# Performance work log

Measured on AMD Instinct MI355X. Metric: run time of the kernel, lower is better.

## Reference

```python
import jax, jax.numpy as jnp
import numpy as np

B, Q, D = 8, 128, 2048
H, HD = 16, 128           # num_heads, head_dim (D == H*HD)
CACHE = 3968              # tokens already in KV cache; CACHE+Q == max_seq_len


def setup_inputs() -> dict:
    key = jax.random.key(0)
    ks = jax.random.split(key, 6)
    x = jax.random.normal(ks[0], (B, Q, D), dtype=jnp.float32)
    k_cache = jax.random.normal(ks[1], (B, H, CACHE, HD), dtype=jnp.float32)
    v_cache = jax.random.normal(ks[2], (B, H, CACHE, HD), dtype=jnp.float32)
    Wqkv = jax.random.normal(ks[3], (D, 3 * D), dtype=jnp.float32) * 0.02
    Wproj = jax.random.normal(ks[4], (D, D), dtype=jnp.float32) * 0.02
    bproj = jnp.zeros((D,), dtype=jnp.float32)
    return {"x": x, "k_cache": k_cache, "v_cache": v_cache,
            "Wqkv": Wqkv, "Wproj": Wproj, "bproj": bproj}


def reference(x, k_cache, v_cache, Wqkv, Wproj, bproj):
    # QKV projection (qkv_bias=False)
    qkv = x @ Wqkv                                   # [B, Q, 3D]
    qkv = qkv.reshape(B, Q, 3, H, HD)
    qkv = jnp.transpose(qkv, (2, 0, 3, 1, 4))        # [3, B, H, Q, HD]
    q, k_new, v_new = qkv[0], qkv[1], qkv[2]
    # KV-cache append (cache_pos + Q == max_seq_len, no roll)
    k_all = jnp.concatenate([k_cache, k_new], axis=2)  # [B, H, K, HD]
    v_all = jnp.concatenate([v_cache, v_new], axis=2)
    K = CACHE + Q
    scale = 1.0 / jnp.sqrt(jnp.float32(HD))
    scores = jnp.einsum('bhqd,bhkd->bhqk', q, k_all) * scale  # [B, H, Q, K]
    # Causal mask aligned to cache (bottom-right): query i sees keys j <= i + (K - Q)
    i = jnp.arange(Q)[:, None]
    j = jnp.arange(K)[None, :]
    mask = j > (i + (K - Q))
    scores = jnp.where(mask, jnp.float32(-jnp.inf), scores)
    attn = jax.nn.softmax(scores, axis=-1)
    out = jnp.einsum('bhqk,bhkd->bhqd', attn, v_all)   # [B, H, Q, HD]
    out = jnp.transpose(out, (0, 2, 1, 3)).reshape(B, Q, D)
    return out @ Wproj + bproj
```

## Files before the change

### kernel.cpp

```cpp
#include <hip/hip_runtime.h>

typedef unsigned int u32;
typedef unsigned short u16;
typedef short s16x8 __attribute__((ext_vector_type(8)));
typedef float f32x4 __attribute__((ext_vector_type(4)));

#define MFMA16(a,b,c) __builtin_amdgcn_mfma_f32_16x16x32_bf16((a),(b),(c),0,0,0)

#define Bb 8
#define Hh 16
#define Qq 128
#define HDd 128
#define Dd 2048
#define CACHE 3968
#define NSPLIT 4
#define SCALE 0.08838834764831845f
#define SM_OFF 8.0f

__device__ __forceinline__ u16 f2bf(float x){
  u32 u = __builtin_bit_cast(u32, x);
  u32 r = ((u >> 16) & 1u) + 0x7fffu;
  return (u16)((u + r) >> 16);
}
__device__ __forceinline__ float bf2f(u16 h){
  return __builtin_bit_cast(float, ((u32)h) << 16);
}
__device__ __forceinline__ u32 pk2(float a, float b){
  return (u32)f2bf(a) | ((u32)f2bf(b) << 16);
}
__device__ __forceinline__ u32 cvtpk(float a, float b){
  u32 r;
  asm("v_cvt_pk_bf16_f32 %0, %1, %2" : "=v"(r) : "v"(a), "v"(b));
  return r;
}
__device__ __forceinline__ float f4c(const float4& v, int j){
  return j==0 ? v.x : j==1 ? v.y : j==2 ? v.z : v.w;
}
__device__ __forceinline__ void gload_lds16(const void* g, void* l){
  __builtin_amdgcn_global_load_lds(
      (const __attribute__((address_space(1))) u32*)g,
      (__attribute__((address_space(3))) u32*)l, 16, 0, 0);
}
__device__ __forceinline__ void lgkm_barrier(){
  asm volatile("s_waitcnt lgkmcnt(0)" ::: "memory");
  __builtin_amdgcn_s_barrier();
}

__global__ void k_cvt(const float* __restrict__ s, u16* __restrict__ d, int n4){
  int i = blockIdx.x * 256 + threadIdx.x;
  if (i < n4){
    float4 v = *(const float4*)(s + (size_t)i * 4);
    *(uint2*)(d + (size_t)i * 4) = make_uint2(pk2(v.x, v.y), pk2(v.z, v.w));
  }
}

__global__ void k_tcvt(const float* __restrict__ s, u16* __restrict__ d, int R, int C){
  __shared__ float t[32][33];
  int tx = threadIdx.x & 31, ty = threadIdx.x >> 5;
  int c0 = blockIdx.x * 32, r0 = blockIdx.y * 32;
#pragma unroll
  for (int i = 0; i < 4; i++)
    t[ty + i*8][tx] = s[(size_t)(r0 + ty + i*8) * C + c0 + tx];
  __syncthreads();
#pragma unroll
  for (int i = 0; i < 4; i++)
    d[(size_t)(c0 + ty + i*8) * R + r0 + tx] = f2bf(t[tx][ty + i*8]);
}

template<int MODE>
__global__ __launch_bounds__(256)
void k_gemm(const u16* __restrict__ A, const u16* __restrict__ Bt, int K, int N,
            u16* __restrict__ oq, u16* __restrict__ ok, u16* __restrict__ ov,
            float* __restrict__ of, const float* __restrict__ bias)
{
  const int m0 = blockIdx.y * 128, n0 = blockIdx.x * 128;
  const int tid = threadIdx.x;
  const int w = tid >> 6, l = tid & 63;
  const int lg = l >> 4, lr = l & 15;
  const int wr = w >> 1, wc = w & 1;

  __shared__ u16 As[2][128 * 32];
  __shared__ u16 Bs[2][128 * 32];

  f32x4 acc[4][4];
#pragma unroll
  for (int i = 0; i < 4; i++)
#pragma unroll
    for (int j = 0; j < 4; j++) acc[i][j] = f32x4{0.f, 0.f, 0.f, 0.f};

  const int nt = K >> 5;

  auto stage = [&](int buf, int t){
    const int k0 = t << 5;
#pragma unroll
    for (int i = 0; i < 2; i++){
      int flat = i * 256 + tid;
      int row = flat >> 2, kq = flat & 3;
      const u16* ga = A + (size_t)(m0 + row) * K + k0 + kq * 8;
      gload_lds16(ga, (char*)&As[buf][0] + (size_t)(i*256 + w*64) * 16);
      const u16* gb = Bt + (size_t)(n0 + row) * K + k0 + kq * 8;
      gload_lds16(gb, (char*)&Bs[buf][0] + (size_t)(i*256 + w*64) * 16);
    }
  };

  stage(0, 0);
  asm volatile("s_waitcnt vmcnt(0)" ::: "memory");
  __syncthreads();

  for (int t = 0; t < nt; ++t){
    const int buf = t & 1;
    if (t + 1 < nt) stage(buf ^ 1, t + 1);
    s16x8 af[4], bfr[4];
#pragma unroll
    for (int i = 0; i < 4; i++){
      int row = wr*64 + i*16 + lr;
      af[i] = *(const s16x8*)&As[buf][row*32 + lg*8];
    }
#pragma unroll
    for (int j = 0; j < 4; j++){
      int col = wc*64 + j*16 + lr;
      bfr[j] = *(const s16x8*)&Bs[buf][col*32 + lg*8];
    }
#pragma unroll
    for (int i = 0; i < 4; i++)
#pragma unroll
      for (int j = 0; j < 4; j++)
        acc[i][j] = MFMA16(af[i], bfr[j], acc[i][j]);
    asm volatile("s_waitcnt vmcnt(0)" ::: "memory");
    __syncthreads();
  }

#pragma unroll
  for (int i = 0; i < 4; i++){
#pragma unroll
    for (int j = 0; j < 4; j++){
#pragma unroll
      for (int r = 0; r < 4; r++){
        int m = m0 + wr*64 + i*16 + lg*4 + r;
        int n = n0 + wc*64 + j*16 + lr;
        float v = acc[i][j][r];
        if (MODE == 0){
          int which = n >> 11;
          int h = (n >> 7) & 15, hd = n & 127;
          int b = m >> 7, qi = m & 127;
          size_t idx = (((size_t)(b * Hh + h)) * Qq + qi) * HDd + hd;
          if (which == 0)      oq[idx] = f2bf(v * SCALE);
          else if (which == 1) ok[idx] = f2bf(v);
          else                 ov[idx] = f2bf(v);
        } else {
          of[(size_t)m * N + n] = v + bias[n];
        }
      }
    }
  }
}

__global__ __launch_bounds__(512, 2)
void k_attn(const float* __restrict__ kc, const float* __restrict__ vc,
            const u16* __restrict__ qw, const u16* __restrict__ knw,
            const u16* __restrict__ vnw, float* __restrict__ opart,
            float2* __restrict__ ml)
{
  const int tid = threadIdx.x;
  const int w = tid >> 6, l = tid & 63;
  const int lg = l >> 4, lr = l & 15;

  __shared__ __align__(16) u16 Ks[2][64 * 136];
  __shared__ u32 Vts[2][128 * 32];

  const int rv = tid & 15, c4v = tid >> 4;

  const int vb = blockIdx.x;
  const int bh = vb >> 2;
  const int sg = vb & 3;

  s16x8 qf[4];
  {
    const u16* qp = qw + (((size_t)bh * Qq + w*16 + lr) * HDd);
#pragma unroll
    for (int kk = 0; kk < 4; kk++) qf[kk] = *(const s16x8*)(qp + kk*32 + lg*8);
  }

  f32x4 acc[8];
#pragma unroll
  for (int i = 0; i < 8; i++) acc[i] = f32x4{0.f, 0.f, 0.f, 0.f};
  float lpart = 0.f;

  const float* kbase = kc + (size_t)bh * CACHE * HDd;
  const float* vbase = vc + (size_t)bh * CACHE * HDd;
  const u16* knb = knw + (size_t)bh * Qq * HDd;
  const u16* vnb = vnw + (size_t)bh * Qq * HDd;

  float4 kreg[4], vreg[4];

  auto loadc = [&](int c){
    if (c < 62){
#pragma unroll
      for (int i = 0; i < 4; i++){
        int flat = tid + i*512;
        int row = flat >> 5, c4 = flat & 31;
        kreg[i] = *(const float4*)(kbase + ((size_t)(c*64 + row)) * HDd + c4*4);
      }
#pragma unroll
      for (int a = 0; a < 4; a++)
        vreg[a] = *(const float4*)(vbase + ((size_t)(c*64 + rv + a*16)) * HDd + c4v*4);
    } else {
#pragma unroll
      for (int i = 0; i < 4; i++){
        int flat = tid + i*512;
        int row = flat >> 5, c4 = flat & 31;
        ushort4 u = *(const ushort4*)(knb + ((size_t)(c*64 + row - CACHE)) * HDd + c4*4);
        kreg[i] = make_float4(bf2f(u.x), bf2f(u.y), bf2f(u.z), bf2f(u.w));
      }
#pragma unroll
      for (int a = 0; a < 4; a++){
        ushort4 u = *(const ushort4*)(vnb + ((size_t)(c*64 + rv + a*16 - CACHE)) * HDd + c4v*4);
        vreg[a] = make_float4(bf2f(u.x), bf2f(u.y), bf2f(u.z), bf2f(u.w));
      }
    }
  };

  auto writeK = [&](int buf){
#pragma unroll
    for (int i = 0; i < 4; i++){
      int flat = tid + i*512;
      int row = flat >> 5, c4 = flat & 31;
      *(uint2*)&Ks[buf][row*136 + c4*4] =
          make_uint2(cvtpk(kreg[i].x, kreg[i].y), cvtpk(kreg[i].z, kreg[i].w));
    }
  };
  auto writeV = [&](int buf){
#pragma unroll
    for (int j = 0; j < 4; j++){
      int col = c4v*4 + j;
      int x2 = (col & 7) << 2;
      Vts[buf][col*32 + (rv ^ x2)]        = cvtpk(f4c(vreg[0], j), f4c(vreg[1], j));
      Vts[buf][col*32 + ((rv + 16) ^ x2)] = cvtpk(f4c(vreg[2], j), f4c(vreg[3], j));
    }
  };

  int cur = 0;
  loadc(sg * 16);
  writeK(0);
  writeV(0);
  __syncthreads();

  for (int cl = 0; cl < 16; ++cl){
    const int c = sg * 16 + cl;
    if (cl + 1 < 16) loadc(c + 1);

    f32x4 s[4];
    __builtin_amdgcn_s_setprio(1);
#pragma unroll
    for (int t = 0; t < 4; t++){
      s[t] = f32x4{0.f, 0.f, 0.f, 0.f};
      const u16* kp = &Ks[cur][(t*16 + lr) * 136];
#pragma unroll
      for (int kk = 0; kk < 4; kk++){
        s16x8 kf = *(const s16x8*)(kp + kk*32 + lg*8);
        s[t] = MFMA16(kf, qf[kk], s[t]);
      }
    }
    __builtin_amdgcn_s_setprio(0);

    if (c >= 62){
      int jn = c*64 - CACHE;
      int qi = w*16 + lr;
#pragma unroll
      for (int t = 0; t < 4; t++)
#pragma unroll
        for (int r = 0; r < 4; r++){
          int kn = jn + t*16 + lg*4 + r;
          if (kn > qi) s[t][r] = -__builtin_inff();
        }
    }

    float ps = 0.f;
#pragma unroll
    for (int t = 0; t < 4; t++)
#pragma unroll
      for (int r = 0; r < 4; r++){
        float p = __expf(s[t][r] - SM_OFF);
        s[t][r] = p;
        ps += p;
      }
    lpart += ps;

    s16x8 pf[2];
    {
      union { uint4 u; s16x8 v; } c0, c1;
      c0.u = make_uint4(cvtpk(s[0][0], s[1][0]), cvtpk(s[0][1], s[1][1]),
                        cvtpk(s[0][2], s[1][2]), cvtpk(s[0][3], s[1][3]));
      c1.u = make_uint4(cvtpk(s[2][0], s[3][0]), cvtpk(s[2][1], s[3][1]),
                        cvtpk(s[2][2], s[3][2]), cvtpk(s[2][3], s[3][3]));
      pf[0] = c0.v;
      pf[1] = c1.v;
    }

    if (cl + 1 < 16) writeK(cur ^ 1);

    __builtin_amdgcn_s_setprio(1);
#pragma unroll
    for (int t = 0; t < 8; t++){
      int col = t*16 + lr;
      const u32* vp = &Vts[cur][col * 32];
#pragma unroll
      for (int kk = 0; kk < 2; kk++){
        s16x8 vf = *(const s16x8*)(vp + ((16*kk + 4*lg) ^ ((col & 7) << 2)));
        acc[t] = MFMA16(vf, pf[kk], acc[t]);
      }
    }
    __builtin_amdgcn_s_setprio(0);

    if (cl + 1 < 16) writeV(cur ^ 1);

    lgkm_barrier();
    cur ^= 1;
  }

  float lsum = lpart;
  lsum += __shfl_xor(lsum, 16);
  lsum += __shfl_xor(lsum, 32);

  float* pbase = opart + (size_t)vb * (Qq * HDd);
  float* Lt = (float*)Ks;
#pragma unroll 1
  for (int half = 0; half < 2; half++){
    if ((w >> 2) == half){
      int ql = (w & 3) * 16 + lr;
#pragma unroll
      for (int t = 0; t < 8; t++)
#pragma unroll
        for (int r = 0; r < 4; r++)
          Lt[ql * 132 + t*16 + lg*4 + r] = acc[t][r];
    }
    __syncthreads();
    {
      int c32 = tid & 31;
#pragma unroll
      for (int j = 0; j < 4; j++){
        int ql = (tid >> 5) + j * 16;
        float4 v = *(const float4*)&Lt[ql * 132 + c32 * 4];
        *(float4*)&pbase[(size_t)(half * 64 + ql) * HDd + c32 * 4] = v;
      }
    }
    __syncthreads();
  }
  if (lg == 0)
    ml[(size_t)vb * Qq + w*16 + lr] = make_float2(SM_OFF, lsum);
}

__global__ __launch_bounds__(256)
void k_comb(const float* __restrict__ opart, const float2* __restrict__ ml,
            u16* __restrict__ ao)
{
  const int bh = blockIdx.x >> 2;
  const int q0 = (blockIdx.x & 3) * 32;
  const int tid = threadIdx.x;

  __shared__ float wgt[32][NSPLIT];
  __shared__ float Ls[32];

  if (tid < 32 * NSPLIT){
    int row = tid >> 2, s = tid & 3;
    float2 v = ml[((size_t)(bh * NSPLIT + s)) * Qq + q0 + row];
    float m = v.x;
    m = fmaxf(m, __shfl_xor(m, 1));
    m = fmaxf(m, __shfl_xor(m, 2));
    float e = __expf(v.x - m);
    float el = e * v.y;
    el += __shfl_xor(el, 1);
    el += __shfl_xor(el, 2);
    wgt[row][s] = e;
    if (s == 0) Ls[row] = el;
  }
  __syncthreads();

  const int cp = tid & 63;
  const int r4 = tid >> 6;
  const int b = bh >> 4, h = bh & 15;
#pragma unroll
  for (int rr = 0; rr < 8; rr++){
    int row = r4 + rr*4;
    float2 a = make_float2(0.f, 0.f);
    const float* pb = opart + ((size_t)(bh * NSPLIT)) * (Qq * HDd)
                            + (size_t)(q0 + row) * HDd + cp*2;
#pragma unroll
    for (int s = 0; s < NSPLIT; s++){
      float2 p = *(const float2*)(pb + (size_t)s * (Qq * HDd));
      float wv = wgt[row][s];
      a.x += wv * p.x;
      a.y += wv * p.y;
    }
    float inv = 1.0f / Ls[row];
    u16* dst = ao + ((size_t)b * Qq + q0 + row) * Dd + h * HDd + cp*2;
    *(u32*)dst = pk2(a.x * inv, a.y * inv);
  }
}

extern "C" void kernel_launch(void* const* d_in, const int* in_sizes, int n_in,
                              void* d_out, int out_size, void* d_ws, size_t ws_size,
                              hipStream_t stream)
{
  const float* x     = (const float*)d_in[0];
  const float* kc    = (const float*)d_in[1];
  const float* vc    = (const float*)d_in[2];
  const float* wqkv  = (const float*)d_in[3];
  const float* wproj = (const float*)d_in[4];
  const float* bproj = (const float*)d_in[5];
  float* out = (float*)d_out;

  char* ws = (char*)d_ws;
  u16* xb  = (u16*)(ws);
  u16* wtq = (u16*)(ws + ((size_t)4  << 20));
  u16* wtp = (u16*)(ws + ((size_t)28 << 20));
  u16* qw  = (u16*)(ws + ((size_t)36 << 20));
  u16* knw = (u16*)(ws + ((size_t)40 << 20));
  u16* vnw = (u16*)(ws + ((size_t)44 << 20));
  u16* aow = (u16*)(ws + ((size_t)48 << 20));
  float* opart = (float*)(ws + ((size_t)52 << 20));
  float2* mlw  = (float2*)(ws + ((size_t)116 << 20));

  k_cvt<<<2048, 256, 0, stream>>>(x, xb, (1024 * 2048) / 4);
  k_tcvt<<<dim3(192, 64), 256, 0, stream>>>(wqkv, wtq, 2048, 6144);
  k_tcvt<<<dim3(64, 64), 256, 0, stream>>>(wproj, wtp, 2048, 2048);
  k_gemm<0><<<dim3(48, 8), 256, 0, stream>>>(xb, wtq, 2048, 6144,
                                             qw, knw, vnw, nullptr, nullptr);
  k_attn<<<Bb * Hh * NSPLIT, 512, 0, stream>>>(kc, vc, qw, knw, vnw, opart, mlw);
  k_comb<<<Bb * Hh * 4, 256, 0, stream>>>(opart, mlw, aow);
  k_gemm<1><<<dim3(16, 8), 256, 0, stream>>>(aow, wtp, 2048, 2048,
                                             nullptr, nullptr, nullptr, out, bproj);
}
```

Baseline: 266.9 us.

## Fuse conversion kernels, halve proj GEMM M-tile, drop setprio in attention

Merges the x conversion and both weight transpose-convert kernels into one k_prep launch to cut launch overhead. Templates the GEMM on M-tile size and runs the output projection with 64-row tiles, doubling its grid from 128 to 256 blocks to fill more CUs. Removes s_setprio hints around the MFMA loops in the attention kernel. The smaller tile lowers per-block reuse, and dropping priority may change how waves interleave.

Result: faster. 253.4 us (-5.1%).

```diff
diff --git a/kernel.cpp b/kernel.cpp
--- a/kernel.cpp
+++ b/kernel.cpp
@@ -46,18 +46,25 @@
   __builtin_amdgcn_s_barrier();
 }
 
-__global__ void k_cvt(const float* __restrict__ s, u16* __restrict__ d, int n4){
-  int i = blockIdx.x * 256 + threadIdx.x;
-  if (i < n4){
-    float4 v = *(const float4*)(s + (size_t)i * 4);
-    *(uint2*)(d + (size_t)i * 4) = make_uint2(pk2(v.x, v.y), pk2(v.z, v.w));
-  }
-}
-
-__global__ void k_tcvt(const float* __restrict__ s, u16* __restrict__ d, int R, int C){
+__global__ __launch_bounds__(256)
+void k_prep(const float* __restrict__ x, u16* __restrict__ xb,
+            const float* __restrict__ wqkv, u16* __restrict__ wtq,
+            const float* __restrict__ wproj, u16* __restrict__ wtp)
+{
   __shared__ float t[32][33];
+  int bid = blockIdx.x;
+  if (bid < 2048){
+    int i = bid * 256 + threadIdx.x;
+    float4 v = *(const float4*)(x + (size_t)i * 4);
+    *(uint2*)(xb + (size_t)i * 4) = make_uint2(pk2(v.x, v.y), pk2(v.z, v.w));
+    return;
+  }
+  bid -= 2048;
+  const float* s; u16* d; int R, C, bx, by;
+  if (bid < 12288){ s = wqkv;  d = wtq; R = 2048; C = 6144; bx = bid % 192; by = bid / 192; }
+  else { bid -= 12288; s = wproj; d = wtp; R = 2048; C = 2048; bx = bid % 64;  by = bid / 64;  }
   int tx = threadIdx.x & 31, ty = threadIdx.x >> 5;
-  int c0 = blockIdx.x * 32, r0 = blockIdx.y * 32;
+  int c0 = bx * 32, r0 = by * 32;
 #pragma unroll
   for (int i = 0; i < 4; i++)
     t[ty + i*8][tx] = s[(size_t)(r0 + ty + i*8) * C + c0 + tx];
@@ -67,37 +74,45 @@
     d[(size_t)(c0 + ty + i*8) * R + r0 + tx] = f2bf(t[tx][ty + i*8]);
 }
 
-template<int MODE>
+template<int MODE, int TM>
 __global__ __launch_bounds__(256)
 void k_gemm(const u16* __restrict__ A, const u16* __restrict__ Bt, int K, int N,
             u16* __restrict__ oq, u16* __restrict__ ok, u16* __restrict__ ov,
             float* __restrict__ of, const float* __restrict__ bias)
 {
-  const int m0 = blockIdx.y * 128, n0 = blockIdx.x * 128;
+  const int m0 = blockIdx.y * TM, n0 = blockIdx.x * 128;
   const int tid = threadIdx.x;
   const int w = tid >> 6, l = tid & 63;
   const int lg = l >> 4, lr = l & 15;
-  const int wr = w >> 1, wc = w & 1;
-
-  __shared__ u16 As[2][128 * 32];
+  const int wr = (TM == 128) ? (w >> 1) : 0;
+  const int wc = (TM == 128) ? (w & 1) : w;
+  constexpr int WN = (TM == 128) ? 64 : 32;
+  constexpr int NJ = WN / 16;
+
+  __shared__ u16 As[2][TM * 32];
   __shared__ u16 Bs[2][128 * 32];
 
-  f32x4 acc[4][4];
+  f32x4 acc[4][NJ];
 #pragma unroll
   for (int i = 0; i < 4; i++)
 #pragma unroll
-    for (int j = 0; j < 4; j++) acc[i][j] = f32x4{0.f, 0.f, 0.f, 0.f};
+    for (int j = 0; j < NJ; j++) acc[i][j] = f32x4{0.f, 0.f, 0.f, 0.f};
 
   const int nt = K >> 5;
 
   auto stage = [&](int buf, int t){
     const int k0 = t << 5;
 #pragma unroll
-    for (int i = 0; i < 2; i++){
+    for (int i = 0; i < TM/64; i++){
       int flat = i * 256 + tid;
       int row = flat >> 2, kq = flat & 3;
       const u16* ga = A + (size_t)(m0 + row) * K + k0 + kq * 8;
       gload_lds16(ga, (char*)&As[buf][0] + (size_t)(i*256 + w*64) * 16);
+    }
+#pragma unroll
+    for (int i = 0; i < 2; i++){
+      int flat = i * 256 + tid;
+      int row = flat >> 2, kq = flat & 3;
       const u16* gb = Bt + (size_t)(n0 + row) * K + k0 + kq * 8;
       gload_lds16(gb, (char*)&Bs[buf][0] + (size_t)(i*256 + w*64) * 16);
     }
@@ -110,21 +125,21 @@
   for (int t = 0; t < nt; ++t){
     const int buf = t & 1;
     if (t + 1 < nt) stage(buf ^ 1, t + 1);
-    s16x8 af[4], bfr[4];
+    s16x8 af[4], bfr[NJ];
 #pragma unroll
     for (int i = 0; i < 4; i++){
       int row = wr*64 + i*16 + lr;
       af[i] = *(const s16x8*)&As[buf][row*32 + lg*8];
     }
 #pragma unroll
-    for (int j = 0; j < 4; j++){
-      int col = wc*64 + j*16 + lr;
+    for (int j = 0; j < NJ; j++){
+      int col = wc*WN + j*16 + lr;
       bfr[j] = *(const s16x8*)&Bs[buf][col*32 + lg*8];
     }
 #pragma unroll
     for (int i = 0; i < 4; i++)
 #pragma unroll
-      for (int j = 0; j < 4; j++)
+      for (int j = 0; j < NJ; j++)
         acc[i][j] = MFMA16(af[i], bfr[j], acc[i][j]);
     asm volatile("s_waitcnt vmcnt(0)" ::: "memory");
     __syncthreads();
@@ -133,11 +148,11 @@
 #pragma unroll
   for (int i = 0; i < 4; i++){
 #pragma unroll
-    for (int j = 0; j < 4; j++){
+    for (int j = 0; j < NJ; j++){
 #pragma unroll
       for (int r = 0; r < 4; r++){
         int m = m0 + wr*64 + i*16 + lg*4 + r;
-        int n = n0 + wc*64 + j*16 + lr;
+        int n = n0 + wc*WN + j*16 + lr;
         float v = acc[i][j][r];
         if (MODE == 0){
           int which = n >> 11;
@@ -250,7 +265,6 @@
     if (cl + 1 < 16) loadc(c + 1);
 
     f32x4 s[4];
-    __builtin_amdgcn_s_setprio(1);
 #pragma unroll
     for (int t = 0; t < 4; t++){
       s[t] = f32x4{0.f, 0.f, 0.f, 0.f};
@@ -261,7 +275,6 @@
         s[t] = MFMA16(kf, qf[kk], s[t]);
       }
     }
-    __builtin_amdgcn_s_setprio(0);
 
     if (c >= 62){
       int jn = c*64 - CACHE;
@@ -299,7 +312,6 @@
 
     if (cl + 1 < 16) writeK(cur ^ 1);
 
-    __builtin_amdgcn_s_setprio(1);
 #pragma unroll
     for (int t = 0; t < 8; t++){
       int col = t*16 + lr;
@@ -310,7 +322,6 @@
         acc[t] = MFMA16(vf, pf[kk], acc[t]);
       }
     }
-    __builtin_amdgcn_s_setprio(0);
 
     if (cl + 1 < 16) writeV(cur ^ 1);
 
@@ -421,13 +432,11 @@
   float* opart = (float*)(ws + ((size_t)52 << 20));
   float2* mlw  = (float2*)(ws + ((size_t)116 << 20));
 
-  k_cvt<<<2048, 256, 0, stream>>>(x, xb, (1024 * 2048) / 4);
-  k_tcvt<<<dim3(192, 64), 256, 0, stream>>>(wqkv, wtq, 2048, 6144);
-  k_tcvt<<<dim3(64, 64), 256, 0, stream>>>(wproj, wtp, 2048, 2048);
-  k_gemm<0><<<dim3(48, 8), 256, 0, stream>>>(xb, wtq, 2048, 6144,
-                                             qw, knw, vnw, nullptr, nullptr);
+  k_prep<<<18432, 256, 0, stream>>>(x, xb, wqkv, wtq, wproj, wtp);
+  k_gemm<0,128><<<dim3(48, 8), 256, 0, stream>>>(xb, wtq, 2048, 6144,
+                                                 qw, knw, vnw, nullptr, nullptr);
   k_attn<<<Bb * Hh * NSPLIT, 512, 0, stream>>>(kc, vc, qw, knw, vnw, opart, mlw);
   k_comb<<<Bb * Hh * 4, 256, 0, stream>>>(opart, mlw, aow);
-  k_gemm<1><<<dim3(16, 8), 256, 0, stream>>>(aow, wtp, 2048, 2048,
-                                             nullptr, nullptr, nullptr, out, bproj);
-}
+  k_gemm<1,64><<<dim3(16, 16), 256, 0, stream>>>(aow, wtp, 2048, 2048,
+                                                 nullptr, nullptr, nullptr, out, bproj);
+}
```
